# Kernel optimization log

Hardware: AMD Instinct MI355X
Metric: run time of the kernel (lower is better)

The kernel has to match this reference:

```python
import jax, jax.numpy as jnp
import numpy as np

N_MELS = 128
N_STATE = 1024
N_HEAD = 8
N_LAYER = 6
STRIDE = 2
HEAD_DIM = N_STATE // N_HEAD  # 128; must equal N_MELS for the rope buffer to broadcast
B = 8
T = 4096


def setup_inputs():
    key = jax.random.key(0)
    ks = iter(jax.random.split(key, 40))
    def rn(shape, s=0.02):
        return jax.random.normal(next(ks), shape, dtype=jnp.float32) * s
    L, D, F = N_LAYER, N_STATE, 4 * N_STATE
    inp = {}
    inp['x'] = jax.random.normal(next(ks), (B, N_MELS, T), dtype=jnp.float32)
    inp['x_len'] = jax.random.randint(next(ks), (B,), T // 2, T + 1)
    inp['conv1_w'] = rn((D, N_MELS, 3))
    inp['conv1_b'] = jnp.zeros((D,), jnp.float32)
    inp['conv2_w'] = rn((D, D, 3))
    inp['conv2_b'] = jnp.zeros((D,), jnp.float32)
    inp['attn_ln_w'] = jnp.ones((L, D), jnp.float32)
    inp['attn_ln_b'] = jnp.zeros((L, D), jnp.float32)
    inp['q_w'] = rn((L, D, D)); inp['q_b'] = jnp.zeros((L, D), jnp.float32)
    inp['k_w'] = rn((L, D, D))
    inp['v_w'] = rn((L, D, D)); inp['v_b'] = jnp.zeros((L, D), jnp.float32)
    inp['out_w'] = rn((L, D, D)); inp['out_b'] = jnp.zeros((L, D), jnp.float32)
    inp['mlp_ln_w'] = jnp.ones((L, D), jnp.float32)
    inp['mlp_ln_b'] = jnp.zeros((L, D), jnp.float32)
    inp['mlp1_w'] = rn((L, F, D)); inp['mlp1_b'] = jnp.zeros((L, F), jnp.float32)
    inp['mlp2_w'] = rn((L, D, F)); inp['mlp2_b'] = jnp.zeros((L, D), jnp.float32)
    return inp


def _ln(x, w, b, eps=1e-5):
    x = x.astype(jnp.float32)
    m = jnp.mean(x, -1, keepdims=True)
    v = jnp.mean((x - m) ** 2, -1, keepdims=True)
    return (x - m) * jax.lax.rsqrt(v + eps) * w + b


def _conv1d(x, w, b, stride):
    # x: [B, Cin, T]; w: [Cout, Cin, K] (torch OIH layout); pad=1
    y = jax.lax.conv_general_dilated(x, w, (stride,), [(1, 1)],
                                     dimension_numbers=('NCH', 'OIH', 'NCH'))
    return y + b[None, :, None]


def reference(x, x_len, conv1_w, conv1_b, conv2_w, conv2_b,
              attn_ln_w, attn_ln_b, q_w, q_b, k_w, v_w, v_b, out_w, out_b,
              mlp_ln_w, mlp_ln_b, mlp1_w, mlp1_b, mlp2_w, mlp2_b):
    Tin = x.shape[-1]
    h = jax.nn.gelu(_conv1d(x, conv1_w, conv1_b, STRIDE), approximate=False)
    h = jax.nn.gelu(_conv1d(h, conv2_w, conv2_b, 2), approximate=False)
    h = jnp.transpose(h, (0, 2, 1))  # [B, S, D]
    S = h.shape[1]

    # non-pad mask over original mel frames, subsampled like the conv stack
    mask = jnp.arange(Tin)[None, :] < x_len[:, None]
    mask = mask[:, (Tin + 1) % 2::2]
    if STRIDE == 2:
        Tm = mask.shape[-1]
        mask = mask[:, (Tm + 1) % 2::2]
    bias = ((1.0 - mask.astype(jnp.float32)) * -1.0e10)[:, None, None, :]  # [B,1,1,S]

    # rotary embedding table (freqs_cis as cos/sin), dim == HEAD_DIM == N_MELS
    half = HEAD_DIM // 2
    freqs = 1.0 / (10000.0 ** (jnp.arange(0, HEAD_DIM, 2, dtype=jnp.float32) / HEAD_DIM))
    ang = jnp.arange(S, dtype=jnp.float32)[:, None] * freqs[None, :]  # [S, half]
    cos = jnp.cos(ang)[None, :, None, :]
    sin = jnp.sin(ang)[None, :, None, :]
    scale = HEAD_DIM ** (-0.25)

    def rot(t):  # t: [B,S,H,HEAD_DIM], interleaved (re, im) pairs
        tr = t.reshape(t.shape[0], t.shape[1], N_HEAD, half, 2)
        re, im = tr[..., 0], tr[..., 1]
        return jnp.stack([re * cos - im * sin, re * sin + im * cos], -1)\
                  .reshape(t.shape[0], t.shape[1], N_HEAD, HEAD_DIM)

    def block(carry, p):
        aw, ab, qw, qb, kw, vw, vb, ow, ob, mw, mb, w1, b1, w2, b2 = p
        y = _ln(carry, aw, ab)
        q = y @ qw.T + qb
        k = y @ kw.T          # key has no bias
        v = y @ vw.T + vb
        Bb, Ss = q.shape[0], q.shape[1]
        q = rot(q.reshape(Bb, Ss, N_HEAD, HEAD_DIM)) * scale
        k = rot(k.reshape(Bb, Ss, N_HEAD, HEAD_DIM)) * scale
        v = v.reshape(Bb, Ss, N_HEAD, HEAD_DIM)
        qk = jnp.einsum('bqhd,bkhd->bhqk', q, k) + bias
        w = jax.nn.softmax(qk.astype(jnp.float32), axis=-1)
        o = jnp.einsum('bhqk,bkhd->bqhd', w, v).reshape(Bb, Ss, N_STATE)
        carry = carry + o @ ow.T + ob
        y = _ln(carry, mw, mb)
        y = jax.nn.gelu(y @ w1.T + b1, approximate=False) @ w2.T + b2
        return carry + y, None

    params = (attn_ln_w, attn_ln_b, q_w, q_b, k_w, v_w, v_b, out_w, out_b,
              mlp_ln_w, mlp_ln_b, mlp1_w, mlp1_b, mlp2_w, mlp2_b)
    h, _ = jax.lax.scan(block, h, params)

    y_len = (x_len + 1) // 2
    if STRIDE == 2:
        y_len = (y_len + 1) // 2
    return h, y_len
```

## Files before the change

kernel.cpp:

```cpp
#include <hip/hip_runtime.h>
#include <hip/hip_bf16.h>
#include <cstdint>
#include <cstddef>


typedef __bf16 bf16_t;
typedef __bf16 bf16x8 __attribute__((ext_vector_type(8)));
typedef __bf16 bf16x4 __attribute__((ext_vector_type(4)));
typedef float  floatx4 __attribute__((ext_vector_type(4)));

#define NB   8
#define NS   1024
#define ND   1024
#define NT   4096
#define NT1  2048

#define MFMA16(a, b, c) __builtin_amdgcn_mfma_f32_16x16x32_bf16(a, b, c, 0, 0, 0)

#define SBAR() do { __builtin_amdgcn_sched_barrier(0); \
                    __builtin_amdgcn_s_barrier();      \
                    __builtin_amdgcn_sched_barrier(0); } while (0)

__device__ __forceinline__ float gelu_f(float x) {
  const float t = 1.5957691216057308f * (x + 0.044715f * x * x * x);
  return x / (1.0f + __expf(-t));
}

__device__ __forceinline__ void gload16(const void* g, void* l) {
  __builtin_amdgcn_global_load_lds(
      (__attribute__((address_space(1))) void*)(const_cast<void*>(g)),
      (__attribute__((address_space(3))) void*)l, 16, 0, 0);
}

enum { EPI_BF16 = 0, EPI_GELU_BF16 = 2, EPI_GELU_F32 = 3, EPI_RES_F32 = 4, EPI_QKV = 5 };

__device__ __forceinline__ void xcd_remap(int& bx, int& by) {
  const int gx = gridDim.x, gy = gridDim.y;
  const int id  = bx + by * gx;
  const int xcd = id & 7;
  const int r   = id >> 3;
  const int cby = (gx * gy) >> 7;
  const int ncx = gx >> 4;
  const int cx  = xcd % ncx, cy = xcd / ncx;
  bx = cx * 16 + (r & 15);
  by = cy * cby + (r >> 4);
}

#define COMPUTE(BC) { \
    const bf16x8 a0 = *(const bf16x8*)(rA + (BC) * 8192 +    0); \
    const bf16x8 a1 = *(const bf16x8*)(rA + (BC) * 8192 + 1024); \
    const bf16x8 a2 = *(const bf16x8*)(rA + (BC) * 8192 + 2048); \
    const bf16x8 a3 = *(const bf16x8*)(rA + (BC) * 8192 + 3072); \
    const bf16x8 b0 = *(const bf16x8*)(rB + (BC) * 8192 +    0); \
    const bf16x8 b1 = *(const bf16x8*)(rB + (BC) * 8192 + 1024); \
    acc[0][0] = MFMA16(a0, b0, acc[0][0]); acc[0][1] = MFMA16(a0, b1, acc[0][1]); \
    acc[1][0] = MFMA16(a1, b0, acc[1][0]); acc[1][1] = MFMA16(a1, b1, acc[1][1]); \
    acc[2][0] = MFMA16(a2, b0, acc[2][0]); acc[2][1] = MFMA16(a2, b1, acc[2][1]); \
    acc[3][0] = MFMA16(a3, b0, acc[3][0]); acc[3][1] = MFMA16(a3, b1, acc[3][1]); \
  }

#define GSTEP(BC, BS) do { \
    gload16(aP, dA + (BS) * 4096); gload16(bP, dB + (BS) * 4096); \
    aP += 32; bP += 32; \
    COMPUTE(BC); \
    asm volatile("s_waitcnt vmcnt(2)" ::: "memory"); \
    SBAR(); \
  } while (0)

template<int EPI>
__global__ __launch_bounds__(512, 4)
void gemm_bt(const bf16_t* __restrict__ A, long lda,
             const bf16_t* __restrict__ Bm, long ldb,
             void* Cv, long ldc,
             const float* __restrict__ bias, const float* res,
             int K, int swz,
             bf16_t* out2, bf16_t* out3, const float* __restrict__ bias2,
             const float2* __restrict__ rtab)
{
  __shared__ bf16_t sA[3][4096];
  __shared__ bf16_t sB[3][4096];
  const int tid  = threadIdx.x;
  const int wid  = tid >> 6;
  const int lane = tid & 63;
  const int lo = lane & 15, g = lane >> 4;
  const int wr = wid >> 2, wc = wid & 3;

  int bx = blockIdx.x, by = blockIdx.y;
  if (swz) xcd_remap(bx, by);
  const int m0 = bx * 128, n0 = by * 128;
  const int NTK = K >> 5;

  const int lrow = lane >> 2;
  const int lcol = 8 * ((lane & 3) ^ ((lane >> 3) & 3));
  const int rslot = 16 * (g ^ ((lo >> 1) & 3));

  const bf16_t* aP = A  + (long)(m0 + wid * 16 + lrow) * lda + lcol;
  const bf16_t* bP = Bm + (long)(n0 + wid * 16 + lrow) * ldb + lcol;
  bf16_t* const dA = &sA[0][wid * 512];
  bf16_t* const dB = &sB[0][wid * 512];
  const char* const rA = (const char*)&sA[0][0] + (wr * 64 + lo) * 64 + rslot;
  const char* const rB = (const char*)&sB[0][0] + (wc * 32 + lo) * 64 + rslot;

  floatx4 acc[4][2] = {};

  gload16(aP, dA);            gload16(bP, dB);
  gload16(aP + 32, dA + 4096); gload16(bP + 32, dB + 4096);
  aP += 64; bP += 64;
  asm volatile("s_waitcnt vmcnt(2)" ::: "memory");
  SBAR();

  int s = 0;
#pragma unroll 1
  for (; s + 5 <= NTK; s += 3) {
    GSTEP(0, 2);
    GSTEP(1, 0);
    GSTEP(2, 1);
  }
#pragma unroll 1
  for (; s < NTK; ++s) {
    if (s + 2 < NTK) {
      const int bs = (s + 2) % 3;
      gload16(aP, dA + bs * 4096); gload16(bP, dB + bs * 4096);
      aP += 32; bP += 32;
    }
    const int bc = s % 3;
    {
      const char* rAd = rA + bc * 8192;
      const char* rBd = rB + bc * 8192;
      const bf16x8 a0 = *(const bf16x8*)(rAd +    0);
      const bf16x8 a1 = *(const bf16x8*)(rAd + 1024);
      const bf16x8 a2 = *(const bf16x8*)(rAd + 2048);
      const bf16x8 a3 = *(const bf16x8*)(rAd + 3072);
      const bf16x8 b0 = *(const bf16x8*)(rBd +    0);
      const bf16x8 b1 = *(const bf16x8*)(rBd + 1024);
      acc[0][0] = MFMA16(a0, b0, acc[0][0]); acc[0][1] = MFMA16(a0, b1, acc[0][1]);
      acc[1][0] = MFMA16(a1, b0, acc[1][0]); acc[1][1] = MFMA16(a1, b1, acc[1][1]);
      acc[2][0] = MFMA16(a2, b0, acc[2][0]); acc[2][1] = MFMA16(a2, b1, acc[2][1]);
      acc[3][0] = MFMA16(a3, b0, acc[3][0]); acc[3][1] = MFMA16(a3, b1, acc[3][1]);
    }
    asm volatile("s_waitcnt vmcnt(0)" ::: "memory");
    SBAR();
  }

  if constexpr (EPI == EPI_QKV) {
    const int sect = n0 >> 10;
#pragma unroll
    for (int ni = 0; ni < 2; ++ni) {
      const int col = n0 + wc * 32 + ni * 16 + lo;
      const int c10 = col & 1023;
      float bvs = 0.0f;
      if (sect == 0) bvs = bias[c10];
      else if (sect == 2) bvs = bias2[c10];
#pragma unroll
      for (int mi = 0; mi < 4; ++mi) {
#pragma unroll
        for (int r = 0; r < 4; ++r) {
          const int row = m0 + wr * 64 + mi * 16 + g * 4 + r;
          const int sr = row & 1023;
          float val = acc[mi][ni][r] + bvs;
          if (sect < 2) {
            const float2 t = rtab[(sr << 6) + ((col & 127) >> 1)];
            const float p = __shfl_xor(val, 1);
            val = val * t.x + p * ((col & 1) ? t.y : -t.y);
            bf16_t* dst = sect ? out2 : (bf16_t*)Cv;
            dst[(long)row * 1024 + c10] = (bf16_t)val;
          } else {
            out3[((long)(row >> 10) << 20) + ((long)(col - 2048) << 10) + sr] = (bf16_t)val;
          }
        }
      }
    }
    return;
  }

#pragma unroll
  for (int ni = 0; ni < 2; ++ni) {
    const int col = n0 + wc * 32 + ni * 16 + lo;
    const float bvs = bias ? bias[col] : 0.0f;
#pragma unroll
    for (int mi = 0; mi < 4; ++mi) {
#pragma unroll
      for (int r = 0; r < 4; ++r) {
        const int row = m0 + wr * 64 + mi * 16 + g * 4 + r;
        float v = acc[mi][ni][r] + bvs;
        if constexpr (EPI == EPI_BF16) {
          ((bf16_t*)Cv)[(long)row * ldc + col] = (bf16_t)v;
        } else if constexpr (EPI == EPI_GELU_BF16) {
          ((bf16_t*)Cv)[(long)row * ldc + col] = (bf16_t)gelu_f(v);
        } else if constexpr (EPI == EPI_GELU_F32) {
          ((float*)Cv)[(long)row * ldc + col] = gelu_f(v);
        } else {
          const long idx = (long)row * ldc + col;
          ((float*)Cv)[idx] = res[idx] + v;
        }
      }
    }
  }
}

__global__ __launch_bounds__(256, 4)
void flash_kernel(const bf16_t* __restrict__ q, const bf16_t* __restrict__ k,
                  const bf16_t* __restrict__ vt, bf16_t* __restrict__ o,
                  const int* __restrict__ xlen)
{
  __shared__ bf16_t sK[2][4096];
  __shared__ bf16_t sV[2][4096];
  __shared__ bf16_t sP[4][512];
  const int tid = threadIdx.x, w = tid >> 6, lane = tid & 63;
  const int lo = lane & 15, g = lane >> 4;
  const int hid = blockIdx.x + (blockIdx.y << 4);
  const int h   = hid & 7;
  const int qx  = (hid >> 3) & 15;
  const int b   = hid >> 7;
  const int q0 = qx * 64 + w * 16;
  const int nv  = xlen[b] >> 2;
  const int nkt = (nv + 31) >> 5;
  const long base = (long)b * 1048576 + (long)h * 128;
  const bf16_t* Qp = q + base;
  const bf16_t* Kp = k + base;
  const bf16_t* Vp = vt + (long)b * 1048576 + ((long)h << 17);

  auto stageKV = [&](int kt, int buf) {
    const int kv0 = kt << 5;
#pragma unroll
    for (int jj = 0; jj < 2; ++jj) {
      const int seg = (w << 1) + jj;
      {
        const int row = (seg << 2) + (lane >> 4);
        const int col = ((lane & 15) << 3) ^ ((row & 7) << 3);
        gload16(Kp + (long)(kv0 + row) * 1024 + col, &sK[buf][seg * 512]);
      }
      {
        const int row = (seg << 4) + (lane >> 2);
        const int col = ((lane & 3) << 3) ^ ((row & 3) << 3);
        gload16(Vp + (long)row * 1024 + kv0 + col, &sV[buf][seg * 512]);
      }
    }
  };

  bf16x8 qf[4];
#pragma unroll
  for (int ks = 0; ks < 4; ++ks)
    qf[ks] = *reinterpret_cast<const bf16x8*>(
        Qp + (long)(q0 + lo) * 1024 + ks * 32 + g * 8);

  floatx4 of[8] = {};
  float m[4], l[4];
#pragma unroll
  for (int r = 0; r < 4; ++r) { m[r] = -1e30f; l[r] = 0.0f; }

  const char* kbase = (const char*)&sK[0][0];
  const char* vbase = (const char*)&sV[0][0];
  char* pbase = (char*)&sP[w][0];
  const int swzK = (lo & 7) << 4;
  const int swzV = (lo & 3) << 4;

  stageKV(0, 0);
  __syncthreads();
  int cur = 0;
#pragma unroll 1
  for (int kt = 0; kt < nkt; ++kt) {
    const int kv0 = kt << 5;
    if (kt + 1 < nkt) stageKV(kt + 1, cur ^ 1);

    floatx4 s[2] = {};
    __builtin_amdgcn_s_setprio(1);
#pragma unroll
    for (int ni = 0; ni < 2; ++ni) {
#pragma unroll
      for (int ks = 0; ks < 4; ++ks) {
        const bf16x8 bv = *reinterpret_cast<const bf16x8*>(
            kbase + cur * 8192 + (ni * 16 + lo) * 256 + ((ks * 64 + (g << 4)) ^ swzK));
        s[ni] = MFMA16(qf[ks], bv, s[ni]);
      }
    }
    __builtin_amdgcn_s_setprio(0);

    float pmv[4];
#pragma unroll
    for (int r = 0; r < 4; ++r) {
      float pm = -1e30f;
#pragma unroll
      for (int ni = 0; ni < 2; ++ni) {
        float val = s[ni][r];
        if (kv0 + ni * 16 + lo >= nv) val = -1e30f;
        pm = fmaxf(pm, val);
      }
      pm = fmaxf(pm, __shfl_xor(pm, 1)); pm = fmaxf(pm, __shfl_xor(pm, 2));
      pm = fmaxf(pm, __shfl_xor(pm, 4)); pm = fmaxf(pm, __shfl_xor(pm, 8));
      pmv[r] = pm;
    }
    const bool skip = __all((pmv[0] <= m[0] + 8.0f) & (pmv[1] <= m[1] + 8.0f) &
                            (pmv[2] <= m[2] + 8.0f) & (pmv[3] <= m[3] + 8.0f));

#pragma unroll
    for (int r = 0; r < 4; ++r) {
      float mn = m[r];
      if (!skip) {
        mn = fmaxf(m[r], pmv[r]);
        const float sc = __expf(m[r] - mn);
        l[r] *= sc;
#pragma unroll
        for (int nd = 0; nd < 8; ++nd) of[nd][r] *= sc;
        m[r] = mn;
      }
      const int qrow = g * 4 + r;
      const int sw = (qrow & 3) << 4;
      float ss = 0.0f;
#pragma unroll
      for (int ni = 0; ni < 2; ++ni) {
        float val = s[ni][r];
        if (kv0 + ni * 16 + lo >= nv) val = -1e30f;
        const float p = __expf(val - mn);
        ss += p;
        *(bf16_t*)(pbase + qrow * 64 + (((ni << 5) + (lo << 1)) ^ sw)) = (bf16_t)p;
      }
      ss += __shfl_xor(ss, 1); ss += __shfl_xor(ss, 2);
      ss += __shfl_xor(ss, 4); ss += __shfl_xor(ss, 8);
      l[r] += ss;
    }

    asm volatile("s_waitcnt lgkmcnt(0)" ::: "memory");
    __builtin_amdgcn_sched_barrier(0);

    __builtin_amdgcn_s_setprio(1);
    {
      const bf16x8 av = *reinterpret_cast<const bf16x8*>(
          pbase + lo * 64 + ((g << 4) ^ swzV));
#pragma unroll
      for (int nd = 0; nd < 8; ++nd) {
        const bf16x8 bv = *reinterpret_cast<const bf16x8*>(
            vbase + cur * 8192 + (nd * 16 + lo) * 64 + ((g << 4) ^ swzV));
        of[nd] = MFMA16(av, bv, of[nd]);
      }
    }
    __builtin_amdgcn_s_setprio(0);
    __syncthreads();
    cur ^= 1;
  }

#pragma unroll
  for (int r = 0; r < 4; ++r) {
    const float inv = 1.0f / l[r];
    const long rb = base + (long)(q0 + g * 4 + r) * 1024;
#pragma unroll
    for (int nd = 0; nd < 8; ++nd)
      o[rb + nd * 16 + lo] = (bf16_t)(of[nd][r] * inv);
  }
}

__global__ __launch_bounds__(256)
void ln_kernel(const float* __restrict__ x, bf16_t* __restrict__ y,
               const float* __restrict__ w, const float* __restrict__ b)
{
  const long row = blockIdx.x;
  const float4 v = reinterpret_cast<const float4*>(x + row * ND)[threadIdx.x];
  float s  = v.x + v.y + v.z + v.w;
  float ss = v.x * v.x + v.y * v.y + v.z * v.z + v.w * v.w;
#pragma unroll
  for (int off = 32; off; off >>= 1) { s += __shfl_down(s, off); ss += __shfl_down(ss, off); }
  __shared__ float sh[8];
  if ((threadIdx.x & 63) == 0) { sh[threadIdx.x >> 6] = s; sh[4 + (threadIdx.x >> 6)] = ss; }
  __syncthreads();
  const float tot  = sh[0] + sh[1] + sh[2] + sh[3];
  const float tot2 = sh[4] + sh[5] + sh[6] + sh[7];
  const float mean = tot * (1.0f / ND);
  const float var  = tot2 * (1.0f / ND) - mean * mean;
  const float rstd = rsqrtf(var + 1e-5f);
  const int i0 = threadIdx.x * 4;
  const float vv[4] = {v.x, v.y, v.z, v.w};
  bf16x4 o;
#pragma unroll
  for (int j = 0; j < 4; ++j)
    o[j] = (bf16_t)((vv[j] - mean) * rstd * w[i0 + j] + b[i0 + j]);
  reinterpret_cast<bf16x4*>(y + row * ND)[threadIdx.x] = o;
}

__global__ __launch_bounds__(256)
void rtab_kernel(float2* __restrict__ tab)
{
  const int idx = blockIdx.x * 256 + threadIdx.x;
  const int s = idx >> 6, i = idx & 63;
  const float freq = __expf((float)i * -0.14391156831212787f);
  float sn, cs;
  sincosf((float)s * freq, &sn, &cs);
  const float sc = 0.29730177875068026f;
  tab[idx] = make_float2(cs * sc, sn * sc);
}

__global__ __launch_bounds__(256)
void im2col1_kernel(const float* __restrict__ x, bf16_t* __restrict__ a)
{
  const long idx = (long)blockIdx.x * 256 + threadIdx.x;
  if (idx >= (long)NB * NT1 * 384) return;
  const int  k = (int)(idx % 384);
  const long m = idx / 384;
  const int i = k / 3, kk = k - 3 * i;
  const int t = (int)(m & (NT1 - 1));
  const int b = (int)(m >> 11);
  const int tt = 2 * t + kk - 1;
  float v = 0.0f;
  if (tt >= 0 && tt < NT) v = x[((long)b * 128 + i) * NT + tt];
  a[idx] = (bf16_t)v;
}

__global__ __launch_bounds__(256)
void im2col2_kernel(const bf16_t* __restrict__ h1, bf16_t* __restrict__ a)
{
  const long idx = (long)blockIdx.x * 256 + threadIdx.x;
  if (idx >= (long)NB * NS * 3072) return;
  const int  k = (int)(idx % 3072);
  const long m = idx / 3072;
  const int i = k / 3, kk = k - 3 * i;
  const int t = (int)(m & (NS - 1));
  const int b = (int)(m >> 10);
  const int tt = 2 * t + kk - 1;
  bf16_t v = (bf16_t)0.0f;
  if (tt >= 0 && tt < NT1) v = h1[((long)b * NT1 + tt) * ND + i];
  a[idx] = v;
}

__global__ void ylen_kernel(const int* __restrict__ xlen, float* __restrict__ ylen)
{
  const int b = threadIdx.x;
  if (b < NB) {
    const int y1 = (xlen[b] + 1) >> 1;
    ylen[b] = (float)((y1 + 1) >> 1);
  }
}

__global__ __launch_bounds__(256)
void cvt_kernel(const float* __restrict__ in, bf16_t* __restrict__ out, long n)
{
  const long i = ((long)blockIdx.x * 256 + threadIdx.x) * 4;
  if (i >= n) return;
  const float4 v = *reinterpret_cast<const float4*>(in + i);
  bf16x4 o;
  o[0] = (bf16_t)v.x; o[1] = (bf16_t)v.y; o[2] = (bf16_t)v.z; o[3] = (bf16_t)v.w;
  *reinterpret_cast<bf16x4*>(out + i) = o;
}

__global__ __launch_bounds__(256)
void cvt_layer_kernel(const float* __restrict__ qw, const float* __restrict__ kw,
                      const float* __restrict__ vw, const float* __restrict__ ow,
                      const float* __restrict__ w1, const float* __restrict__ w2,
                      bf16_t* __restrict__ wqkv, bf16_t* __restrict__ wo,
                      bf16_t* __restrict__ w1b, bf16_t* __restrict__ w2b)
{
  const long i = ((long)blockIdx.x * 256 + threadIdx.x) * 4;
  const float* src; bf16_t* dst;
  if (i < 3145728) {
    dst = wqkv + i;
    if (i < 1048576)      { src = qw + i; }
    else if (i < 2097152) { src = kw + (i - 1048576); }
    else                  { src = vw + (i - 2097152); }
  } else if (i < 4194304) { src = ow + (i - 3145728); dst = wo  + (i - 3145728); }
  else if (i < 8388608)   { src = w1 + (i - 4194304); dst = w1b + (i - 4194304); }
  else                    { src = w2 + (i - 8388608); dst = w2b + (i - 8388608); }
  const float4 v = *reinterpret_cast<const float4*>(src);
  bf16x4 o;
  o[0] = (bf16_t)v.x; o[1] = (bf16_t)v.y; o[2] = (bf16_t)v.z; o[3] = (bf16_t)v.w;
  *reinterpret_cast<bf16x4*>(dst) = o;
}

extern "C" void kernel_launch(void* const* d_in, const int* in_sizes, int n_in,
                              void* d_out, int out_size, void* d_ws, size_t ws_size,
                              hipStream_t stream)
{
  const float* x         = (const float*)d_in[0];
  const int*   x_len     = (const int*)  d_in[1];
  const float* conv1_w   = (const float*)d_in[2];
  const float* conv1_b   = (const float*)d_in[3];
  const float* conv2_w   = (const float*)d_in[4];
  const float* conv2_b   = (const float*)d_in[5];
  const float* attn_ln_w = (const float*)d_in[6];
  const float* attn_ln_b = (const float*)d_in[7];
  const float* q_w   = (const float*)d_in[8];
  const float* q_b   = (const float*)d_in[9];
  const float* k_w   = (const float*)d_in[10];
  const float* v_w   = (const float*)d_in[11];
  const float* v_b   = (const float*)d_in[12];
  const float* out_w = (const float*)d_in[13];
  const float* out_b = (const float*)d_in[14];
  const float* mlp_ln_w = (const float*)d_in[15];
  const float* mlp_ln_b = (const float*)d_in[16];
  const float* mlp1_w = (const float*)d_in[17];
  const float* mlp1_b = (const float*)d_in[18];
  const float* mlp2_w = (const float*)d_in[19];
  const float* mlp2_b = (const float*)d_in[20];
  float* outp = (float*)d_out;
  (void)in_sizes; (void)n_in; (void)out_size;

  const long MB = 1024L * 1024;
  char* ws = (char*)d_ws;
  size_t off = 0;
  auto alloc = [&](size_t bytes) -> char* {
    char* p = ws + off;
    off += (bytes + 255) & ~(size_t)255;
    return p;
  };
  bf16_t* ybuf  = (bf16_t*)alloc(16 * MB);
  bf16_t* qbuf  = (bf16_t*)alloc(16 * MB);
  char*   R     = alloc(64 * MB);
  char*   wA    = alloc(25 * MB);
  const size_t required = off;

  bf16_t* a1  = ybuf;
  bf16_t* h1  = qbuf;
  bf16_t* a2  = (bf16_t*)(R + 16 * MB);
  bf16_t* c2w = (bf16_t*)wA;
  bf16_t* c1w = (bf16_t*)(wA + 8 * MB);
  float2* rtab = (float2*)(wA + 6 * MB);
  bf16_t* wqkv = (bf16_t*)wA;
  bf16_t* wo   = (bf16_t*)(wA + 6 * MB + 512 * 1024);
  bf16_t* w1b  = (bf16_t*)(wA + 9 * MB);
  bf16_t* w2b  = (bf16_t*)(wA + 17 * MB);
  bf16_t* kbuf = (bf16_t*)R;
  bf16_t* vt   = (bf16_t*)(R + 16 * MB);
  bf16_t* hid  = (bf16_t*)R;

  if (required > ws_size) {
    ylen_kernel<<<dim3(1), 64, 0, stream>>>(x_len, outp + 8L * 1024 * 1024);
    return;
  }

  auto cvt = [&](const float* in, bf16_t* o, long n) {
    cvt_kernel<<<dim3((unsigned)(n / 1024)), 256, 0, stream>>>(in, o, n);
  };

  rtab_kernel<<<dim3(256), 256, 0, stream>>>(rtab);

  cvt(conv1_w, c1w, 1024L * 384);
  cvt(conv2_w, c2w, 1024L * 3072);
  im2col1_kernel<<<dim3((unsigned)((16384L * 384) / 256)), 256, 0, stream>>>(x, a1);
  gemm_bt<EPI_GELU_BF16><<<dim3(128, 8), 512, 0, stream>>>(
      a1, 384, c1w, 384, h1, 1024, conv1_b, nullptr, 384, 1,
      nullptr, nullptr, nullptr, nullptr);
  im2col2_kernel<<<dim3((unsigned)((8192L * 3072) / 256)), 256, 0, stream>>>(h1, a2);
  gemm_bt<EPI_GELU_F32><<<dim3(64, 8), 512, 0, stream>>>(
      a2, 3072, c2w, 3072, outp , 1024, conv2_b, nullptr, 3072, 1,
      nullptr, nullptr, nullptr, nullptr);

  float* carry = outp;

  for (int l = 0; l < 6; ++l) {
    cvt_layer_kernel<<<dim3(12288), 256, 0, stream>>>(
        q_w + (long)l * 1048576, k_w + (long)l * 1048576, v_w + (long)l * 1048576,
        out_w + (long)l * 1048576, mlp1_w + (long)l * 4194304, mlp2_w + (long)l * 4194304,
        wqkv, wo, w1b, w2b);

    ln_kernel<<<dim3(8192), 256, 0, stream>>>(carry, ybuf, attn_ln_w + l * 1024, attn_ln_b + l * 1024);

    gemm_bt<EPI_QKV><<<dim3(64, 24), 512, 0, stream>>>(
        ybuf, 1024, wqkv, 1024, qbuf, 1024,
        q_b + l * 1024, nullptr, 1024, 1, kbuf, vt, v_b + l * 1024, rtab);

    flash_kernel<<<dim3(16, 64), 256, 0, stream>>>(qbuf, kbuf, vt, qbuf, x_len);

    gemm_bt<EPI_RES_F32><<<dim3(64, 8), 512, 0, stream>>>(
        qbuf, 1024, wo, 1024, carry, 1024,
        out_b + l * 1024, carry, 1024, 1, nullptr, nullptr, nullptr, nullptr);

    ln_kernel<<<dim3(8192), 256, 0, stream>>>(carry, ybuf, mlp_ln_w + l * 1024, mlp_ln_b + l * 1024);

    gemm_bt<EPI_GELU_BF16><<<dim3(64, 32), 512, 0, stream>>>(
        ybuf, 1024, w1b, 1024, hid, 4096,
        mlp1_b + (long)l * 4096, nullptr, 1024, 1, nullptr, nullptr, nullptr, nullptr);
    gemm_bt<EPI_RES_F32><<<dim3(64, 8), 512, 0, stream>>>(
        hid, 4096, w2b, 4096, carry, 1024,
        mlp2_b + l * 1024, carry, 4096, 1, nullptr, nullptr, nullptr, nullptr);
  }

  ylen_kernel<<<dim3(1), 64, 0, stream>>>(x_len, outp + 8L * 1024 * 1024);
}
```

Baseline: 2.650 ms.

## Switch GEMM mainloop to double-buffered 64-wide K tiles with split loads

```diff
diff --git a/kernel.cpp b/kernel.cpp
--- a/kernel.cpp
+++ b/kernel.cpp
@@ -46,24 +46,34 @@
   by = cy * cby + (r >> 4);
 }
 
-#define COMPUTE(BC) { \
-    const bf16x8 a0 = *(const bf16x8*)(rA + (BC) * 8192 +    0); \
-    const bf16x8 a1 = *(const bf16x8*)(rA + (BC) * 8192 + 1024); \
-    const bf16x8 a2 = *(const bf16x8*)(rA + (BC) * 8192 + 2048); \
-    const bf16x8 a3 = *(const bf16x8*)(rA + (BC) * 8192 + 3072); \
-    const bf16x8 b0 = *(const bf16x8*)(rB + (BC) * 8192 +    0); \
-    const bf16x8 b1 = *(const bf16x8*)(rB + (BC) * 8192 + 1024); \
+#define COMPUTE2(BUF, H) { \
+    const char* rAd = rA + (BUF) * 16384 + (H) * 8192; \
+    const char* rBd = rB + (BUF) * 16384 + (H) * 8192; \
+    const bf16x8 a0 = *(const bf16x8*)(rAd +    0); \
+    const bf16x8 a1 = *(const bf16x8*)(rAd + 1024); \
+    const bf16x8 a2 = *(const bf16x8*)(rAd + 2048); \
+    const bf16x8 a3 = *(const bf16x8*)(rAd + 3072); \
+    const bf16x8 b0 = *(const bf16x8*)(rBd +    0); \
+    const bf16x8 b1 = *(const bf16x8*)(rBd + 1024); \
     acc[0][0] = MFMA16(a0, b0, acc[0][0]); acc[0][1] = MFMA16(a0, b1, acc[0][1]); \
     acc[1][0] = MFMA16(a1, b0, acc[1][0]); acc[1][1] = MFMA16(a1, b1, acc[1][1]); \
     acc[2][0] = MFMA16(a2, b0, acc[2][0]); acc[2][1] = MFMA16(a2, b1, acc[2][1]); \
     acc[3][0] = MFMA16(a3, b0, acc[3][0]); acc[3][1] = MFMA16(a3, b1, acc[3][1]); \
   }
 
-#define GSTEP(BC, BS) do { \
-    gload16(aP, dA + (BS) * 4096); gload16(bP, dB + (BS) * 4096); \
-    aP += 32; bP += 32; \
-    COMPUTE(BC); \
-    asm volatile("s_waitcnt vmcnt(2)" ::: "memory"); \
+#define KSTEP(BUF, SNEXT_OK) do { \
+    if (SNEXT_OK) { \
+      gload16(aP,      dA + ((BUF) ^ 1) * 8192);        \
+      gload16(aP + 32, dA + ((BUF) ^ 1) * 8192 + 4096); \
+    } \
+    COMPUTE2(BUF, 0); \
+    if (SNEXT_OK) { \
+      gload16(bP,      dB + ((BUF) ^ 1) * 8192);        \
+      gload16(bP + 32, dB + ((BUF) ^ 1) * 8192 + 4096); \
+      aP += 64; bP += 64; \
+    } \
+    COMPUTE2(BUF, 1); \
+    asm volatile("s_waitcnt vmcnt(0)" ::: "memory"); \
     SBAR(); \
   } while (0)
 
@@ -77,8 +87,8 @@
              bf16_t* out2, bf16_t* out3, const float* __restrict__ bias2,
              const float2* __restrict__ rtab)
 {
-  __shared__ bf16_t sA[3][4096];
-  __shared__ bf16_t sB[3][4096];
+  __shared__ bf16_t sA[2][8192];
+  __shared__ bf16_t sB[2][8192];
   const int tid  = threadIdx.x;
   const int wid  = tid >> 6;
   const int lane = tid & 63;
@@ -88,7 +98,7 @@
   int bx = blockIdx.x, by = blockIdx.y;
   if (swz) xcd_remap(bx, by);
   const int m0 = bx * 128, n0 = by * 128;
-  const int NTK = K >> 5;
+  const int NTK = K >> 6;
 
   const int lrow = lane >> 2;
   const int lcol = 8 * ((lane & 3) ^ ((lane >> 3) & 3));
@@ -103,43 +113,16 @@
 
   floatx4 acc[4][2] = {};
 
-  gload16(aP, dA);            gload16(bP, dB);
-  gload16(aP + 32, dA + 4096); gload16(bP + 32, dB + 4096);
+  gload16(aP,      dA);         gload16(aP + 32, dA + 4096);
+  gload16(bP,      dB);         gload16(bP + 32, dB + 4096);
   aP += 64; bP += 64;
-  asm volatile("s_waitcnt vmcnt(2)" ::: "memory");
+  asm volatile("s_waitcnt vmcnt(0)" ::: "memory");
   SBAR();
 
-  int s = 0;
 #pragma unroll 1
-  for (; s + 5 <= NTK; s += 3) {
-    GSTEP(0, 2);
-    GSTEP(1, 0);
-    GSTEP(2, 1);
-  }
-#pragma unroll 1
-  for (; s < NTK; ++s) {
-    if (s + 2 < NTK) {
-      const int bs = (s + 2) % 3;
-      gload16(aP, dA + bs * 4096); gload16(bP, dB + bs * 4096);
-      aP += 32; bP += 32;
-    }
-    const int bc = s % 3;
-    {
-      const char* rAd = rA + bc * 8192;
-      const char* rBd = rB + bc * 8192;
-      const bf16x8 a0 = *(const bf16x8*)(rAd +    0);
-      const bf16x8 a1 = *(const bf16x8*)(rAd + 1024);
-      const bf16x8 a2 = *(const bf16x8*)(rAd + 2048);
-      const bf16x8 a3 = *(const bf16x8*)(rAd + 3072);
-      const bf16x8 b0 = *(const bf16x8*)(rBd +    0);
-      const bf16x8 b1 = *(const bf16x8*)(rBd + 1024);
-      acc[0][0] = MFMA16(a0, b0, acc[0][0]); acc[0][1] = MFMA16(a0, b1, acc[0][1]);
-      acc[1][0] = MFMA16(a1, b0, acc[1][0]); acc[1][1] = MFMA16(a1, b1, acc[1][1]);
-      acc[2][0] = MFMA16(a2, b0, acc[2][0]); acc[2][1] = MFMA16(a2, b1, acc[2][1]);
-      acc[3][0] = MFMA16(a3, b0, acc[3][0]); acc[3][1] = MFMA16(a3, b1, acc[3][1]);
-    }
-    asm volatile("s_waitcnt vmcnt(0)" ::: "memory");
-    SBAR();
+  for (int s = 0; s < NTK; s += 2) {
+    KSTEP(0, (s + 1 < NTK));
+    KSTEP(1, (s + 2 < NTK));
   }
 
   if constexpr (EPI == EPI_QKV) {
```

Measured after the change: 2.602 ms (median of 2 runs). Within noise of the previous version (-1.8%).
